# Optimization experiments

Hardware: AMD Instinct MI355X
Metric: run time of the kernel (lower is better)

The kernel has to match this reference:

```python
import jax, jax.numpy as jnp
import numpy as np

SCALE = 16.0 / 8.0  # alpha / r

def setup_inputs() -> dict:
    key = jax.random.key(0)
    ks = jax.random.split(key, 6)
    B, S, IN_F, OUT_F, E, R = 4, 2048, 2048, 2048, 4, 8
    x = jax.random.normal(ks[0], (B, S, IN_F), dtype=jnp.float32)
    base_w = jax.random.normal(ks[1], (OUT_F, IN_F), dtype=jnp.float32) * (1.0 / np.sqrt(IN_F))
    base_b = jax.random.normal(ks[2], (OUT_F,), dtype=jnp.float32) * 0.02
    A = jax.random.normal(ks[3], (E, R, IN_F), dtype=jnp.float32) * (1.0 / np.sqrt(IN_F))
    Bm = jax.random.normal(ks[4], (E, OUT_F, R), dtype=jnp.float32) * 0.02
    router_w = jax.random.normal(ks[5], (E, IN_F), dtype=jnp.float32) * (1.0 / np.sqrt(IN_F))
    return {"x": x, "base_w": base_w, "base_b": base_b, "A": A, "B": Bm, "router_w": router_w}

def reference(x, base_w, base_b, A, B, router_w):
    # base linear: (B,S,out_f)
    base_out = jnp.einsum('bsi,oi->bso', x, base_w) + base_b
    # router + softmax gates over experts: (B,S,E)
    router_logits = jnp.einsum('bsi,ei->bse', x, router_w)
    gates = jax.nn.softmax(router_logits, axis=-1)
    # routing == 'weighted': use soft gates directly
    # LoRA: down-project to rank r per expert, then up-project
    proj_r = jnp.einsum('bsi,eri->bser', x, A)        # (B,S,E,r)
    lora_out = jnp.einsum('bser,eor->bseo', proj_r, B)  # (B,S,E,out_f)
    # gate-weighted sum over experts, scaled by alpha/r
    lora_mix = jnp.einsum('bseo,bse->bso', lora_out, gates * SCALE)
    return base_out + lora_mix
```

## Files before the change

kernel.cpp:

```cpp
#include <hip/hip_runtime.h>
#include <hip/hip_bf16.h>
#include <stdint.h>

#define M_ROWS 8192
#define KDIM   2048
#define NDIM   2048
#define SCALE_F 2.0f

typedef __attribute__((ext_vector_type(8))) short  bf16x8;
typedef __attribute__((ext_vector_type(4))) float  f32x4;
typedef __attribute__((ext_vector_type(8))) unsigned short u16x8;

__device__ __forceinline__ unsigned short f2bf(float f) {
    unsigned u = __float_as_uint(f);
    unsigned r = (u + 0x7fffu + ((u >> 16) & 1u)) >> 16;
    return (unsigned short)r;
}

#define GLOAD_LDS16(gptr, lptr) \
    __builtin_amdgcn_global_load_lds((const __attribute__((address_space(1))) void*)(gptr), \
                                     (__attribute__((address_space(3))) void*)(lptr), 16, 0, 0)

__global__ __launch_bounds__(256) void k_convert(
    const float* __restrict__ x,
    const float* __restrict__ bw,
    const float* __restrict__ A,
    const float* __restrict__ rw,
    const float* __restrict__ Bm,
    unsigned short* __restrict__ xb,
    unsigned short* __restrict__ wb,
    unsigned short* __restrict__ W36,
    unsigned short* __restrict__ Bc)
{
    const int t = blockIdx.x * 256 + threadIdx.x;
    const int nthr = gridDim.x * 256;

    for (int i = t; i < (M_ROWS * KDIM / 8); i += nthr) {
        float4 v0 = *(const float4*)(x + (size_t)i * 8);
        float4 v1 = *(const float4*)(x + (size_t)i * 8 + 4);
        u16x8 o = { f2bf(v0.x), f2bf(v0.y), f2bf(v0.z), f2bf(v0.w),
                    f2bf(v1.x), f2bf(v1.y), f2bf(v1.z), f2bf(v1.w) };
        *(u16x8*)(xb + (size_t)i * 8) = o;
    }
    for (int i = t; i < (NDIM * KDIM / 8); i += nthr) {
        float4 v0 = *(const float4*)(bw + (size_t)i * 8);
        float4 v1 = *(const float4*)(bw + (size_t)i * 8 + 4);
        u16x8 o = { f2bf(v0.x), f2bf(v0.y), f2bf(v0.z), f2bf(v0.w),
                    f2bf(v1.x), f2bf(v1.y), f2bf(v1.z), f2bf(v1.w) };
        *(u16x8*)(wb + (size_t)i * 8) = o;
    }
    if (t < 48 * 2048 / 8) {
        const int row = (t * 8) >> 11, col = (t * 8) & 2047;
        u16x8 o;
        if (row < 36) {
            const float* src = (row < 32) ? (A + (size_t)row * 2048 + col)
                                          : (rw + (size_t)(row - 32) * 2048 + col);
            float4 v0 = *(const float4*)(src);
            float4 v1 = *(const float4*)(src + 4);
            o = (u16x8){ f2bf(v0.x), f2bf(v0.y), f2bf(v0.z), f2bf(v0.w),
                         f2bf(v1.x), f2bf(v1.y), f2bf(v1.z), f2bf(v1.w) };
        } else {
            o = (u16x8){0, 0, 0, 0, 0, 0, 0, 0};
        }
        *(u16x8*)(W36 + (size_t)t * 8) = o;
    }
    if (t < 4 * 2048) {
        const int e = t >> 11, o = t & 2047;
        const float* src = Bm + ((size_t)e * 2048 + o) * 8;
        float4 v0 = *(const float4*)(src);
        float4 v1 = *(const float4*)(src + 4);
        u16x8 ov = { f2bf(v0.x), f2bf(v0.y), f2bf(v0.z), f2bf(v0.w),
                     f2bf(v1.x), f2bf(v1.y), f2bf(v1.z), f2bf(v1.w) };
        *(u16x8*)(Bc + (size_t)o * 32 + e * 8) = ov;
    }
}

__global__ __launch_bounds__(64) void k_proj(
    const unsigned short* __restrict__ xb,
    const unsigned short* __restrict__ W36,
    unsigned short* __restrict__ Wg)
{
    const int l = threadIdx.x;
    const int l15 = l & 15, l16h = l >> 4;
    const int row0 = blockIdx.x * 16;

    const unsigned short* pa = xb + (size_t)(row0 + l15) * KDIM + l16h * 8;
    const unsigned short* pb0 = W36 + (size_t)(0 * 16 + l15) * KDIM + l16h * 8;
    const unsigned short* pb1 = W36 + (size_t)(1 * 16 + l15) * KDIM + l16h * 8;
    const unsigned short* pb2 = W36 + (size_t)(2 * 16 + l15) * KDIM + l16h * 8;

    f32x4 acc[3];
#pragma unroll
    for (int n = 0; n < 3; ++n) acc[n] = (f32x4){0.f, 0.f, 0.f, 0.f};

#pragma unroll 4
    for (int kt = 0; kt < KDIM / 32; ++kt) {
        bf16x8 a = *(const bf16x8*)(pa + kt * 32);
        bf16x8 b0 = *(const bf16x8*)(pb0 + kt * 32);
        bf16x8 b1 = *(const bf16x8*)(pb1 + kt * 32);
        bf16x8 b2 = *(const bf16x8*)(pb2 + kt * 32);
        acc[0] = __builtin_amdgcn_mfma_f32_16x16x32_bf16(a, b0, acc[0], 0, 0, 0);
        acc[1] = __builtin_amdgcn_mfma_f32_16x16x32_bf16(a, b1, acc[1], 0, 0, 0);
        acc[2] = __builtin_amdgcn_mfma_f32_16x16x32_bf16(a, b2, acc[2], 0, 0, 0);
    }

#pragma unroll
    for (int j = 0; j < 4; ++j) {
        const int base = l & 48;
        float lg0 = __shfl(acc[2][j], base + 0);
        float lg1 = __shfl(acc[2][j], base + 1);
        float lg2 = __shfl(acc[2][j], base + 2);
        float lg3 = __shfl(acc[2][j], base + 3);
        float mx = fmaxf(fmaxf(lg0, lg1), fmaxf(lg2, lg3));
        float e0 = __expf(lg0 - mx), e1 = __expf(lg1 - mx);
        float e2 = __expf(lg2 - mx), e3 = __expf(lg3 - mx);
        float inv = SCALE_F / (e0 + e1 + e2 + e3);
        float g0 = e0 * inv, g1 = e1 * inv, g2 = e2 * inv, g3 = e3 * inv;

        const int row = row0 + l16h * 4 + j;
#pragma unroll
        for (int n = 0; n < 2; ++n) {
            const int cn = n * 16 + l15;
            const int e = cn >> 3;
            float g = (e == 0) ? g0 : (e == 1) ? g1 : (e == 2) ? g2 : g3;
            Wg[(size_t)row * 32 + cn] = f2bf(g * acc[n][j]);
        }
    }
}

#define PH(JB, AH, BH, DO_ARD, DO_BRD, STAGE_STMT, CKPT_STMT) do {             \
    if (DO_ARD) {                                                              \
      _Pragma("unroll") for (int mi = 0; mi < 4; ++mi) {                       \
        afr[mi][0] = *(const bf16x8*)&S[(JB)*16384 + (AH)*8192 + mi*1024 + aoff0]; \
        afr[mi][1] = *(const bf16x8*)&S[(JB)*16384 + (AH)*8192 + mi*1024 + aoff1]; \
      }                                                                        \
    }                                                                          \
    if (DO_BRD) {                                                              \
      _Pragma("unroll") for (int ni = 0; ni < 2; ++ni) {                       \
        bfr[BH][ni][0] = *(const bf16x8*)&Sb[(JB)*16384 + (BH)*8192 + ni*1024 + boff0]; \
        bfr[BH][ni][1] = *(const bf16x8*)&Sb[(JB)*16384 + (BH)*8192 + ni*1024 + boff1]; \
      }                                                                        \
    }                                                                          \
    STAGE_STMT                                                                 \
    CKPT_STMT                                                                  \
    __builtin_amdgcn_s_barrier();                                              \
    __builtin_amdgcn_s_setprio(1);                                             \
    _Pragma("unroll") for (int mi = 0; mi < 4; ++mi)                           \
      _Pragma("unroll") for (int ni = 0; ni < 2; ++ni) {                       \
        acc[(AH)*4+mi][(BH)*2+ni] = __builtin_amdgcn_mfma_f32_16x16x32_bf16(   \
            afr[mi][0], bfr[BH][ni][0], acc[(AH)*4+mi][(BH)*2+ni], 0, 0, 0);   \
        acc[(AH)*4+mi][(BH)*2+ni] = __builtin_amdgcn_mfma_f32_16x16x32_bf16(   \
            afr[mi][1], bfr[BH][ni][1], acc[(AH)*4+mi][(BH)*2+ni], 0, 0, 0);   \
      }                                                                        \
    __builtin_amdgcn_s_setprio(0);                                             \
    __builtin_amdgcn_s_barrier();                                              \
  } while (0)

__global__ __launch_bounds__(512, 2) void k_gemm(
    const unsigned short* __restrict__ xb,
    const unsigned short* __restrict__ wb,
    const unsigned short* __restrict__ Wg,
    const unsigned short* __restrict__ Bc,
    const float* __restrict__ bias,
    float* __restrict__ out)
{
    extern __shared__ unsigned short S[];
    unsigned short* Sb = S + 32768;

    const int tid = threadIdx.x;
    const int l = tid & 63, w = tid >> 6;
    const int l15 = l & 15, l16h = l >> 4, l7 = l & 7;
    const int wr = w >> 2, wc = w & 3;

    const int bid = blockIdx.x;
    const int tile = (bid & 7) * 32 + (bid >> 3);
    const int mt = tile >> 3, nt = tile & 7;
    const int m0 = mt * 256, n0 = nt * 256;

    const int aoff0 = (wr * 64 + l15) * 64 + ((l16h ^ l7) << 3);
    const int aoff1 = (wr * 64 + l15) * 64 + (((4 + l16h) ^ l7) << 3);
    const int boff0 = (wc * 32 + l15) * 64 + ((l16h ^ l7) << 3);
    const int boff1 = (wc * 32 + l15) * 64 + (((4 + l16h) ^ l7) << 3);

    const int st_row = w * 8 + (l >> 3);
    const int st_col = ((l & 7) ^ (l >> 3)) * 8;
    const unsigned short* gA0 = xb + (size_t)(m0 + st_row) * KDIM + st_col;
    const unsigned short* gB0 = wb + (size_t)(n0 + st_row) * KDIM + st_col;
    const int sw = w * 512;

    auto stageA = [&](int t, int h) {
        unsigned short* lp = S + ((t & 1) * 16384 + h * 8192 + sw);
        const unsigned short* gp = gA0 + (size_t)h * 128 * KDIM + t * 64;
        GLOAD_LDS16(gp, lp);
        GLOAD_LDS16(gp + (size_t)64 * KDIM, lp + 4096);
    };
    auto stageB = [&](int t, int h) {
        unsigned short* lp = Sb + ((t & 1) * 16384 + h * 8192 + sw);
        const unsigned short* gp = gB0 + (size_t)h * 128 * KDIM + t * 64;
        GLOAD_LDS16(gp, lp);
        GLOAD_LDS16(gp + (size_t)64 * KDIM, lp + 4096);
    };

    f32x4 acc[8][4];
#pragma unroll
    for (int m = 0; m < 8; ++m)
#pragma unroll
        for (int n = 0; n < 4; ++n)
            acc[m][n] = (f32x4){0.f, 0.f, 0.f, 0.f};
    bf16x8 afr[4][2];
    bf16x8 bfr[2][2][2];

    stageA(0, 0); stageA(0, 1); stageB(0, 0); stageB(0, 1);
    stageB(1, 0); stageA(1, 0);
    asm volatile("s_waitcnt vmcnt(4)" ::: "memory");
    __builtin_amdgcn_s_barrier();

#pragma unroll 2
    for (int j = 0; j < 32; ++j) {
        const int jb = j & 1;
        PH(jb, 0, 0, 1, 1, { if (j < 31) stageB(j + 1, 1); }, );
        PH(jb, 0, 1, 0, 1, { if (j < 31) stageA(j + 1, 1); }, );
        PH(jb, 1, 0, 1, 0, { if (j < 30) stageB(j + 2, 0); }, );
        PH(jb, 1, 1, 0, 0, { if (j < 30) stageA(j + 2, 0); },
           { if (j < 30) { asm volatile("s_waitcnt vmcnt(4)" ::: "memory"); }
             else        { asm volatile("s_waitcnt vmcnt(0)" ::: "memory"); } });
    }

    {
        const int lw_row = w * 16 + (l >> 2);
        const int lw_col = (l & 3) * 8;
        unsigned short* lpA = S + sw;
        const unsigned short* gpA = Wg + (size_t)(m0 + lw_row) * 32 + lw_col;
        GLOAD_LDS16(gpA, lpA);
        GLOAD_LDS16(gpA + (size_t)128 * 32, lpA + 4096);
        unsigned short* lpB = Sb + sw;
        const unsigned short* gpB = Bc + (size_t)(n0 + lw_row) * 32 + lw_col;
        GLOAD_LDS16(gpB, lpB);
        GLOAD_LDS16(gpB + (size_t)128 * 32, lpB + 4096);
    }
    asm volatile("s_waitcnt vmcnt(0)" ::: "memory");
    __builtin_amdgcn_s_barrier();

#pragma unroll
    for (int m = 0; m < 8; ++m) {
        bf16x8 af = *(const bf16x8*)&S[((m >> 2) * 128 + wr * 64 + (m & 3) * 16 + l15) * 32 + l16h * 8];
#pragma unroll
        for (int n = 0; n < 4; ++n) {
            bf16x8 bf = *(const bf16x8*)&Sb[((n >> 1) * 128 + wc * 32 + (n & 1) * 16 + l15) * 32 + l16h * 8];
            acc[m][n] = __builtin_amdgcn_mfma_f32_16x16x32_bf16(af, bf, acc[m][n], 0, 0, 0);
        }
    }

#pragma unroll
    for (int n = 0; n < 4; ++n) {
        const int cn = n0 + (n >> 1) * 128 + wc * 32 + (n & 1) * 16 + l15;
        const float bv = bias[cn];
#pragma unroll
        for (int m = 0; m < 8; ++m) {
            const int rm = m0 + (m >> 2) * 128 + wr * 64 + (m & 3) * 16 + l16h * 4;
#pragma unroll
            for (int jj = 0; jj < 4; ++jj)
                out[(size_t)(rm + jj) * NDIM + cn] = acc[m][n][jj] + bv;
        }
    }
}

extern "C" void kernel_launch(void* const* d_in, const int* in_sizes, int n_in,
                              void* d_out, int out_size, void* d_ws, size_t ws_size,
                              hipStream_t stream) {
    const float* x      = (const float*)d_in[0];
    const float* base_w = (const float*)d_in[1];
    const float* base_b = (const float*)d_in[2];
    const float* A      = (const float*)d_in[3];
    const float* Bm     = (const float*)d_in[4];
    const float* rw     = (const float*)d_in[5];
    float* out = (float*)d_out;

    char* ws = (char*)d_ws;
    unsigned short* xb  = (unsigned short*)(ws);
    unsigned short* wb  = (unsigned short*)(ws + 33554432);
    unsigned short* W36 = (unsigned short*)(ws + 33554432 + 8388608);
    unsigned short* Wg  = (unsigned short*)(ws + 33554432 + 8388608 + 196608);
    unsigned short* Bc  = (unsigned short*)(ws + 33554432 + 8388608 + 196608 + 524288);

    k_convert<<<dim3(2048), dim3(256), 0,      stream>>>(x, base_w, A, rw, Bm, xb, wb, W36, Bc);
    k_proj   <<<dim3(512),  dim3(64),  0,      stream>>>(xb, W36, Wg);
    k_gemm   <<<dim3(256),  dim3(512), 131072, stream>>>(xb, wb, Wg, Bc, base_b, out);
}
```

Before: 218.9 us.

## Fuse x bf16 conversion into router/LoRA projection kernel and reorder GEMM phases

The fp32-to-bf16 conversion of x moves out of the convert kernel and into the projection kernel. That kernel now reads fp32 x once, writes bf16 xb and computes the rank/router projections from the same registers, which removes one full pass over x and a separate read of xb. The projection kernel uses 4 waves that each cover a quarter of K and reduces their partial sums through LDS to raise parallelism. The GEMM main loop is restructured so fragment reads are issued earlier, before barriers, and the phase order is changed (1,1 before 1,0) with the next B fragment prefetched at the end of each iteration. The convert grid is shrunk to match the smaller remaining work.

```diff
diff --git a/kernel.cpp b/kernel.cpp
--- a/kernel.cpp
+++ b/kernel.cpp
@@ -22,12 +22,10 @@
                                      (__attribute__((address_space(3))) void*)(lptr), 16, 0, 0)
 
 __global__ __launch_bounds__(256) void k_convert(
-    const float* __restrict__ x,
     const float* __restrict__ bw,
     const float* __restrict__ A,
     const float* __restrict__ rw,
     const float* __restrict__ Bm,
-    unsigned short* __restrict__ xb,
     unsigned short* __restrict__ wb,
     unsigned short* __restrict__ W36,
     unsigned short* __restrict__ Bc)
@@ -35,13 +33,6 @@
     const int t = blockIdx.x * 256 + threadIdx.x;
     const int nthr = gridDim.x * 256;
 
-    for (int i = t; i < (M_ROWS * KDIM / 8); i += nthr) {
-        float4 v0 = *(const float4*)(x + (size_t)i * 8);
-        float4 v1 = *(const float4*)(x + (size_t)i * 8 + 4);
-        u16x8 o = { f2bf(v0.x), f2bf(v0.y), f2bf(v0.z), f2bf(v0.w),
-                    f2bf(v1.x), f2bf(v1.y), f2bf(v1.z), f2bf(v1.w) };
-        *(u16x8*)(xb + (size_t)i * 8) = o;
-    }
     for (int i = t; i < (NDIM * KDIM / 8); i += nthr) {
         float4 v0 = *(const float4*)(bw + (size_t)i * 8);
         float4 v1 = *(const float4*)(bw + (size_t)i * 8 + 4);
@@ -75,27 +66,39 @@
     }
 }
 
-__global__ __launch_bounds__(64) void k_proj(
-    const unsigned short* __restrict__ xb,
+__global__ __launch_bounds__(256) void k_proj(
+    const float* __restrict__ x,
     const unsigned short* __restrict__ W36,
+    unsigned short* __restrict__ xb,
     unsigned short* __restrict__ Wg)
 {
-    const int l = threadIdx.x;
+    __shared__ float red[3][4][64][4];
+
+    const int tid = threadIdx.x;
+    const int l = tid & 63, w = tid >> 6;
     const int l15 = l & 15, l16h = l >> 4;
     const int row0 = blockIdx.x * 16;
-
-    const unsigned short* pa = xb + (size_t)(row0 + l15) * KDIM + l16h * 8;
-    const unsigned short* pb0 = W36 + (size_t)(0 * 16 + l15) * KDIM + l16h * 8;
-    const unsigned short* pb1 = W36 + (size_t)(1 * 16 + l15) * KDIM + l16h * 8;
-    const unsigned short* pb2 = W36 + (size_t)(2 * 16 + l15) * KDIM + l16h * 8;
+    const int kbase = w * 512;
+
+    const float* pa = x + (size_t)(row0 + l15) * KDIM + kbase + l16h * 8;
+    unsigned short* pxb = xb + (size_t)(row0 + l15) * KDIM + kbase + l16h * 8;
+    const unsigned short* pb0 = W36 + (size_t)(0 * 16 + l15) * KDIM + kbase + l16h * 8;
+    const unsigned short* pb1 = W36 + (size_t)(1 * 16 + l15) * KDIM + kbase + l16h * 8;
+    const unsigned short* pb2 = W36 + (size_t)(2 * 16 + l15) * KDIM + kbase + l16h * 8;
 
     f32x4 acc[3];
 #pragma unroll
     for (int n = 0; n < 3; ++n) acc[n] = (f32x4){0.f, 0.f, 0.f, 0.f};
 
 #pragma unroll 4
-    for (int kt = 0; kt < KDIM / 32; ++kt) {
-        bf16x8 a = *(const bf16x8*)(pa + kt * 32);
+    for (int kt = 0; kt < 16; ++kt) {
+        float4 va0 = *(const float4*)(pa + kt * 32);
+        float4 va1 = *(const float4*)(pa + kt * 32 + 4);
+        bf16x8 a = { (short)f2bf(va0.x), (short)f2bf(va0.y),
+                     (short)f2bf(va0.z), (short)f2bf(va0.w),
+                     (short)f2bf(va1.x), (short)f2bf(va1.y),
+                     (short)f2bf(va1.z), (short)f2bf(va1.w) };
+        *(bf16x8*)(pxb + kt * 32) = a;
         bf16x8 b0 = *(const bf16x8*)(pb0 + kt * 32);
         bf16x8 b1 = *(const bf16x8*)(pb1 + kt * 32);
         bf16x8 b2 = *(const bf16x8*)(pb2 + kt * 32);
@@ -105,56 +108,66 @@
     }
 
 #pragma unroll
-    for (int j = 0; j < 4; ++j) {
-        const int base = l & 48;
-        float lg0 = __shfl(acc[2][j], base + 0);
-        float lg1 = __shfl(acc[2][j], base + 1);
-        float lg2 = __shfl(acc[2][j], base + 2);
-        float lg3 = __shfl(acc[2][j], base + 3);
-        float mx = fmaxf(fmaxf(lg0, lg1), fmaxf(lg2, lg3));
-        float e0 = __expf(lg0 - mx), e1 = __expf(lg1 - mx);
-        float e2 = __expf(lg2 - mx), e3 = __expf(lg3 - mx);
-        float inv = SCALE_F / (e0 + e1 + e2 + e3);
-        float g0 = e0 * inv, g1 = e1 * inv, g2 = e2 * inv, g3 = e3 * inv;
-
-        const int row = row0 + l16h * 4 + j;
-#pragma unroll
-        for (int n = 0; n < 2; ++n) {
-            const int cn = n * 16 + l15;
-            const int e = cn >> 3;
-            float g = (e == 0) ? g0 : (e == 1) ? g1 : (e == 2) ? g2 : g3;
-            Wg[(size_t)row * 32 + cn] = f2bf(g * acc[n][j]);
+    for (int n = 0; n < 3; ++n)
+#pragma unroll
+        for (int j = 0; j < 4; ++j)
+            red[n][w][l][j] = acc[n][j];
+    __syncthreads();
+
+    if (w == 0) {
+#pragma unroll
+        for (int n = 0; n < 3; ++n)
+#pragma unroll
+            for (int j = 0; j < 4; ++j)
+                acc[n][j] = red[n][0][l][j] + red[n][1][l][j]
+                          + red[n][2][l][j] + red[n][3][l][j];
+
+#pragma unroll
+        for (int j = 0; j < 4; ++j) {
+            const int base = l & 48;
+            float lg0 = __shfl(acc[2][j], base + 0);
+            float lg1 = __shfl(acc[2][j], base + 1);
+            float lg2 = __shfl(acc[2][j], base + 2);
+            float lg3 = __shfl(acc[2][j], base + 3);
+            float mx = fmaxf(fmaxf(lg0, lg1), fmaxf(lg2, lg3));
+            float e0 = __expf(lg0 - mx), e1 = __expf(lg1 - mx);
+            float e2 = __expf(lg2 - mx), e3 = __expf(lg3 - mx);
+            float inv = SCALE_F / (e0 + e1 + e2 + e3);
+            float g0 = e0 * inv, g1 = e1 * inv, g2 = e2 * inv, g3 = e3 * inv;
+
+            const int row = row0 + l16h * 4 + j;
+#pragma unroll
+            for (int n = 0; n < 2; ++n) {
+                const int cn = n * 16 + l15;
+                const int e = cn >> 3;
+                float g = (e == 0) ? g0 : (e == 1) ? g1 : (e == 2) ? g2 : g3;
+                Wg[(size_t)row * 32 + cn] = f2bf(g * acc[n][j]);
+            }
         }
     }
 }
 
-#define PH(JB, AH, BH, DO_ARD, DO_BRD, STAGE_STMT, CKPT_STMT) do {             \
-    if (DO_ARD) {                                                              \
-      _Pragma("unroll") for (int mi = 0; mi < 4; ++mi) {                       \
-        afr[mi][0] = *(const bf16x8*)&S[(JB)*16384 + (AH)*8192 + mi*1024 + aoff0]; \
-        afr[mi][1] = *(const bf16x8*)&S[(JB)*16384 + (AH)*8192 + mi*1024 + aoff1]; \
-      }                                                                        \
-    }                                                                          \
-    if (DO_BRD) {                                                              \
-      _Pragma("unroll") for (int ni = 0; ni < 2; ++ni) {                       \
-        bfr[BH][ni][0] = *(const bf16x8*)&Sb[(JB)*16384 + (BH)*8192 + ni*1024 + boff0]; \
-        bfr[BH][ni][1] = *(const bf16x8*)&Sb[(JB)*16384 + (BH)*8192 + ni*1024 + boff1]; \
-      }                                                                        \
-    }                                                                          \
-    STAGE_STMT                                                                 \
-    CKPT_STMT                                                                  \
-    __builtin_amdgcn_s_barrier();                                              \
+#define RD_A(C, H) do { _Pragma("unroll") for (int mi = 0; mi < 4; ++mi) {     \
+      afr[mi][0] = *(const bf16x8*)&S[(C)*16384 + (H)*8192 + mi*1024 + aoff0]; \
+      afr[mi][1] = *(const bf16x8*)&S[(C)*16384 + (H)*8192 + mi*1024 + aoff1]; \
+    } } while (0)
+
+#define RD_B(C, H) do { _Pragma("unroll") for (int ni = 0; ni < 2; ++ni) {     \
+      bfr[H][ni][0] = *(const bf16x8*)&Sb[(C)*16384 + (H)*8192 + ni*1024 + boff0]; \
+      bfr[H][ni][1] = *(const bf16x8*)&Sb[(C)*16384 + (H)*8192 + ni*1024 + boff1]; \
+    } } while (0)
+
+#define MFMA16(AH, BH) do {                                                    \
     __builtin_amdgcn_s_setprio(1);                                             \
-    _Pragma("unroll") for (int mi = 0; mi < 4; ++mi)                           \
-      _Pragma("unroll") for (int ni = 0; ni < 2; ++ni) {                       \
-        acc[(AH)*4+mi][(BH)*2+ni] = __builtin_amdgcn_mfma_f32_16x16x32_bf16(   \
-            afr[mi][0], bfr[BH][ni][0], acc[(AH)*4+mi][(BH)*2+ni], 0, 0, 0);   \
-        acc[(AH)*4+mi][(BH)*2+ni] = __builtin_amdgcn_mfma_f32_16x16x32_bf16(   \
-            afr[mi][1], bfr[BH][ni][1], acc[(AH)*4+mi][(BH)*2+ni], 0, 0, 0);   \
-      }                                                                        \
+    _Pragma("unroll") for (int kk = 0; kk < 2; ++kk)                           \
+      _Pragma("unroll") for (int mi = 0; mi < 4; ++mi)                         \
+        _Pragma("unroll") for (int ni = 0; ni < 2; ++ni)                       \
+          acc[(AH)*4+mi][(BH)*2+ni] = __builtin_amdgcn_mfma_f32_16x16x32_bf16( \
+            afr[mi][kk], bfr[BH][ni][kk], acc[(AH)*4+mi][(BH)*2+ni], 0, 0, 0); \
     __builtin_amdgcn_s_setprio(0);                                             \
-    __builtin_amdgcn_s_barrier();                                              \
   } while (0)
+
+#define BAR() __builtin_amdgcn_s_barrier()
 
 __global__ __launch_bounds__(512, 2) void k_gemm(
     const unsigned short* __restrict__ xb,
@@ -213,17 +226,27 @@
     stageA(0, 0); stageA(0, 1); stageB(0, 0); stageB(0, 1);
     stageB(1, 0); stageA(1, 0);
     asm volatile("s_waitcnt vmcnt(4)" ::: "memory");
-    __builtin_amdgcn_s_barrier();
+    BAR();
+    RD_B(0, 0);
 
 #pragma unroll 2
     for (int j = 0; j < 32; ++j) {
-        const int jb = j & 1;
-        PH(jb, 0, 0, 1, 1, { if (j < 31) stageB(j + 1, 1); }, );
-        PH(jb, 0, 1, 0, 1, { if (j < 31) stageA(j + 1, 1); }, );
-        PH(jb, 1, 0, 1, 0, { if (j < 30) stageB(j + 2, 0); }, );
-        PH(jb, 1, 1, 0, 0, { if (j < 30) stageA(j + 2, 0); },
-           { if (j < 30) { asm volatile("s_waitcnt vmcnt(4)" ::: "memory"); }
-             else        { asm volatile("s_waitcnt vmcnt(0)" ::: "memory"); } });
+        const int c = j & 1, d = c ^ 1;
+        RD_A(c, 0);
+        if (j < 31) stageB(j + 1, 1);
+        BAR(); MFMA16(0, 0); BAR();
+        RD_B(c, 1);
+        if (j < 31) stageA(j + 1, 1);
+        BAR(); MFMA16(0, 1); BAR();
+        RD_A(c, 1);
+        if (j < 30) stageB(j + 2, 0);
+        BAR(); MFMA16(1, 1); BAR();
+        if (j < 30) stageA(j + 2, 0);
+        if (j < 30)      { asm volatile("s_waitcnt vmcnt(4)" ::: "memory"); }
+        else if (j == 30){ asm volatile("s_waitcnt vmcnt(0)" ::: "memory"); }
+        BAR(); MFMA16(1, 0);
+        if (j < 31) RD_B(d, 0);
+        BAR();
     }
 
     {
@@ -239,7 +262,7 @@
         GLOAD_LDS16(gpB + (size_t)128 * 32, lpB + 4096);
     }
     asm volatile("s_waitcnt vmcnt(0)" ::: "memory");
-    __builtin_amdgcn_s_barrier();
+    BAR();
 
 #pragma unroll
     for (int m = 0; m < 8; ++m) {
@@ -283,7 +306,7 @@
     unsigned short* Wg  = (unsigned short*)(ws + 33554432 + 8388608 + 196608);
     unsigned short* Bc  = (unsigned short*)(ws + 33554432 + 8388608 + 196608 + 524288);
 
-    k_convert<<<dim3(2048), dim3(256), 0,      stream>>>(x, base_w, A, rw, Bm, xb, wb, W36, Bc);
-    k_proj   <<<dim3(512),  dim3(64),  0,      stream>>>(xb, W36, Wg);
-    k_gemm   <<<dim3(256),  dim3(512), 131072, stream>>>(xb, wb, Wg, Bc, base_b, out);
-}
+    k_convert<<<dim3(512), dim3(256), 0,      stream>>>(base_w, A, rw, Bm, wb, W36, Bc);
+    k_proj   <<<dim3(512), dim3(256), 0,      stream>>>(x, W36, xb, Wg);
+    k_gemm   <<<dim3(256), dim3(512), 131072, stream>>>(xb, wb, Wg, Bc, base_b, out);
+}
```

Result: faster. 206.7 us (-5.6%).
